# Optimization experiments

Hardware: AMD Instinct MI355X
Metric: run time of the kernel (lower is better)

The kernel has to match this reference:

```python
import jax, jax.numpy as jnp
import numpy as np

B, D, G, L = 8, 128, 2048, 24
GF = G // 2 + 1  # rfft bins
EPS = 1e-5


def setup_inputs() -> dict:
    key = jax.random.key(0)
    ks = jax.random.split(key, 6)
    x = jax.random.normal(ks[0], (B, D, G), dtype=jnp.float32)
    Phi_f = jax.random.normal(ks[1], (L, GF), dtype=jnp.float32) * 0.1
    Theta = jax.random.normal(ks[2], (L, D, D), dtype=jnp.float32) * (1.0 / np.sqrt(D))
    ln_gamma = jnp.ones((D,), dtype=jnp.float32)
    ln_beta = jnp.zeros((D,), dtype=jnp.float32)
    fc1_w = jax.random.normal(ks[3], (2 * D, D), dtype=jnp.float32) * (1.0 / np.sqrt(D))
    fc1_b = jnp.zeros((2 * D,), dtype=jnp.float32)
    fc2_w = jax.random.normal(ks[4], (D, 2 * D), dtype=jnp.float32) * (1.0 / np.sqrt(2 * D))
    fc2_b = jnp.zeros((D,), dtype=jnp.float32)
    return {
        'x': x, 'Phi_f': Phi_f, 'Theta': Theta,
        'ln_gamma': ln_gamma, 'ln_beta': ln_beta,
        'fc1_w': fc1_w, 'fc1_b': fc1_b, 'fc2_w': fc2_w, 'fc2_b': fc2_b,
    }


def reference(x, Phi_f, Theta, ln_gamma, ln_beta, fc1_w, fc1_b, fc2_w, fc2_b):
    # x: (B, D, G). LayerNorm over the lifting (channel) dim D.
    mean = jnp.mean(x, axis=1, keepdims=True)
    var = jnp.var(x, axis=1, keepdims=True)
    z = (x - mean) * jax.lax.rsqrt(var + EPS)
    z = z * ln_gamma[None, :, None] + ln_beta[None, :, None]

    # Spectral convolution with each Hilbert filter.
    Xf = jnp.fft.rfft(z, axis=-1)                       # (B, D, GF) complex
    Uf = Xf[:, :, None, :] * jnp.conj(Phi_f)[None, None]  # (B, D, L, GF)
    U = jnp.fft.irfft(Uf, n=G, axis=-1)                 # (B, D, L, G)

    # Per-filter channel mixing then reduction over filters:
    # einsum('bdln,lhd->bhln') followed by sum over l, fused:
    S = jnp.einsum('bdlg,lhd->bhg', U, Theta)           # (B, D, G)

    # Pointwise MLP (Conv1d kernel_size=1 == channel matmul).
    H = jnp.einsum('hd,bdg->bhg', fc1_w, S) + fc1_b[None, :, None]
    H = jax.nn.gelu(H, approximate=False)
    out = jnp.einsum('dh,bhg->bdg', fc2_w, H) + fc2_b[None, :, None]
    return x + out
```

## Files before the change

kernel.cpp:

```cpp
#include <hip/hip_runtime.h>
#include <math.h>


#define B_   8
#define D_   128
#define G_   2048
#define L_   24
#define GF_  1025
#define BD_  1024
#define DD_  16384
#define GH_  1024
#define CF_  1026
#define MF_  1088
#define NF_  2048

#define PA_CV0 256
#define PA_TT0 322
#define PA_WF0 578
#define PA_WI0 1666
#define PA_END 2690

#define G1_NB  544
#define G1_END 4768

typedef __attribute__((ext_vector_type(8))) short  short8v;
typedef __attribute__((ext_vector_type(4))) float  float4v;

union FU { float f; unsigned int u; };
union V8 { short8v v; ushort u[8]; };
union V4 { uint2 p; ushort u[4]; };

static __device__ __forceinline__ float bf2f(ushort h) {
    FU v; v.u = ((unsigned int)h) << 16; return v.f;
}
static __device__ __forceinline__ ushort f2bf(float f) {
    FU v; v.f = f;
    unsigned int r = v.u + 0x7fffu + ((v.u >> 16) & 1u);
    return (ushort)(r >> 16);
}
static __device__ __forceinline__ void async16(const void* g, void* l) {
    __builtin_amdgcn_global_load_lds(
        (const __attribute__((address_space(1))) void*)g,
        (__attribute__((address_space(3))) void*)l, 16, 0, 0);
}
static __device__ __forceinline__ int is_f32(const unsigned int* graw) {
    return graw[0] == 0x3F800000u;
}

__global__ __launch_bounds__(256) void k_pre(
        const void* __restrict__ x_raw,  const void* __restrict__ th_raw,
        const unsigned int* __restrict__ graw, const void* __restrict__ be_raw,
        const void* __restrict__ w1_raw, const void* __restrict__ b1_raw,
        const void* __restrict__ w2_raw, const void* __restrict__ b2_raw,
        ushort* __restrict__ z,  ushort* __restrict__ wf,
        ushort* __restrict__ wi, ushort* __restrict__ thT,
        ushort* __restrict__ w1c, ushort* __restrict__ b1c,
        ushort* __restrict__ w2c, ushort* __restrict__ b2c) {
    __shared__ ushort T[L_][72];
    __shared__ float red[2][256];
    __shared__ float mi[2][64];
    int bid = blockIdx.x, tid = threadIdx.x;

    if (bid < PA_CV0) {
        int fl = is_f32(graw);
        int b  = bid >> 5;
        int g0 = (bid & 31) * 64;
        int gi = tid & 63, dq = tid >> 6;
        int g  = g0 + gi;
        int d0 = dq * 32;
        float vals[32];
        float s = 0.f, ss = 0.f;
        if (fl) {
            const float* xp = (const float*)x_raw + (size_t)(b * D_ + d0) * G_ + g;
            #pragma unroll 8
            for (int d = 0; d < 32; ++d) {
                float v = xp[(size_t)d * G_];
                vals[d] = v; s += v; ss += v * v;
            }
        } else {
            const ushort* xp = (const ushort*)x_raw + (size_t)(b * D_ + d0) * G_ + g;
            #pragma unroll 8
            for (int d = 0; d < 32; ++d) {
                float v = bf2f(xp[(size_t)d * G_]);
                vals[d] = v; s += v; ss += v * v;
            }
        }
        red[0][tid] = s; red[1][tid] = ss;
        __syncthreads();
        if (tid < 64) {
            float S  = red[0][tid] + red[0][tid + 64] + red[0][tid + 128] +
                       red[0][tid + 192];
            float SS = red[1][tid] + red[1][tid + 64] + red[1][tid + 128] +
                       red[1][tid + 192];
            float mean = S * (1.f / D_);
            float var  = SS * (1.f / D_) - mean * mean;
            mi[0][tid] = mean;
            mi[1][tid] = rsqrtf(var + 1e-5f);
        }
        __syncthreads();
        float mean = mi[0][gi], inv = mi[1][gi];
        ushort* zp = z + (size_t)(g & 1) * (BD_ * GH_) +
                     (size_t)(b * D_ + d0) * GH_ + (g >> 1);
        if (fl) {
            const float* gp = (const float*)graw + d0;
            const float* bp = (const float*)be_raw + d0;
            #pragma unroll 8
            for (int d = 0; d < 32; ++d) {
                float o = (vals[d] - mean) * inv * gp[d] + bp[d];
                zp[(size_t)d * GH_] = f2bf(o);
            }
        } else {
            const ushort* gp = (const ushort*)graw + d0;
            const ushort* bp = (const ushort*)be_raw + d0;
            #pragma unroll 8
            for (int d = 0; d < 32; ++d) {
                float o = (vals[d] - mean) * inv * bf2f(gp[d]) + bf2f(bp[d]);
                zp[(size_t)d * GH_] = f2bf(o);
            }
        }
    } else if (bid < PA_TT0) {
        int fl = is_f32(graw);
        int lb = bid - PA_CV0;
        const void* src; ushort* dst; int n, rel;
        if (lb < 32)       { src = w1_raw; dst = w1c; n = 32768; rel = lb; }
        else if (lb == 32) { src = b1_raw; dst = b1c; n = 256;   rel = 0; }
        else if (lb < 65)  { src = w2_raw; dst = w2c; n = 32768; rel = lb - 33; }
        else               { src = b2_raw; dst = b2c; n = 128;   rel = 0; }
        int i0 = rel * 1024 + tid * 4;
        if (fl) {
            const float* s = (const float*)src;
            #pragma unroll
            for (int j = 0; j < 4; ++j) {
                int k = i0 + j;
                if (k < n) dst[k] = f2bf(s[k]);
            }
        } else {
            const ushort* s = (const ushort*)src;
            #pragma unroll
            for (int j = 0; j < 4; ++j) {
                int k = i0 + j;
                if (k < n) dst[k] = s[k];
            }
        }
    } else if (bid < PA_WF0) {
        int fl = is_f32(graw);
        int hd0 = (bid - PA_TT0) * 64;
        if (tid < 192) {
            int l = tid >> 3, c8 = tid & 7;
            V8 o;
            if (fl) {
                const float* tp = (const float*)th_raw + (size_t)l * DD_ +
                                  hd0 + c8 * 8;
                float4v a0 = *(const float4v*)tp;
                float4v a1 = *(const float4v*)(tp + 4);
                #pragma unroll
                for (int j = 0; j < 4; ++j) {
                    o.u[j] = f2bf(a0[j]); o.u[4 + j] = f2bf(a1[j]);
                }
            } else {
                o.v = *(const short8v*)((const ushort*)th_raw +
                                        (size_t)l * DD_ + hd0 + c8 * 8);
            }
            *(short8v*)&T[l][c8 * 8] = o.v;
        }
        __syncthreads();
        int hdl = tid & 63, part = tid >> 6;
        V8 o;
        #pragma unroll
        for (int j = 0; j < 8; ++j) {
            int l = part * 8 + j;
            o.u[j] = (l < L_) ? T[l][hdl] : (ushort)0;
        }
        *(short8v*)(thT + (size_t)(hd0 + hdl) * 32 + part * 8) = o.v;
    } else if (bid < PA_WI0) {
        int c  = bid - PA_WF0;
        int g0 = tid * 4;
        V4 v;
        if (c >= CF_) {
            #pragma unroll
            for (int j = 0; j < 4; ++j) v.u[j] = 0;
        } else {
            int f = c >> 1, im = c & 1;
            #pragma unroll
            for (int j = 0; j < 4; ++j) {
                int g = g0 + j;
                int r = (f * g) & (GH_ - 1);
                float th = (float)r * 6.135923151542565e-3f;
                v.u[j] = f2bf(im ? -__sinf(th) : __cosf(th));
            }
        }
        *(uint2*)(wf + (size_t)c * GH_ + g0) = v.p;
    } else {
        int g = bid - PA_WI0;
        for (int ch = tid; ch < MF_ / 8; ch += 256) {
            int c0 = ch * 8;
            V8 v;
            #pragma unroll
            for (int j = 0; j < 8; ++j) {
                int c = c0 + j;
                if (c >= CF_) { v.u[j] = 0; continue; }
                int f = c >> 1, im = c & 1;
                float a = (f == 0 || f == GH_ / 2) ? (1.f / 2048.f)
                                                   : (1.f / 1024.f);
                int r = (f * g) & (GH_ - 1);
                float th = (float)r * 6.135923151542565e-3f;
                v.u[j] = f2bf(im ? -a * __sinf(th) : a * __cosf(th));
            }
            *(short8v*)(wi + (size_t)g * MF_ + c0) = v.v;
        }
    }
}

__global__ __launch_bounds__(256, 4) void k_g1(
        const ushort* __restrict__ wf, const ushort* __restrict__ z,
        ushort* __restrict__ zft,
        const void* __restrict__ phi_raw, const unsigned int* __restrict__ graw,
        const ushort* __restrict__ thT, ushort* __restrict__ M) {
    __shared__ ushort As[2][64 * 64];
    __shared__ ushort Bs[2][64 * 64];
    __shared__ ushort Aph[16][40];
    int bid = blockIdx.x, tid = threadIdx.x;
    int w = tid >> 6, lane = tid & 63;
    int lr = lane & 15, q = lane >> 4;

    if (bid < G1_NB) {
        int m0 = (bid >> 5) * 64;
        int n0 = (bid & 31) * 64;
        int wm = (w & 1) * 32, wn = (w >> 1) * 32;
        int rl = lane >> 3, c8 = (lane & 7) ^ rl;
        int t0 = w * 2, t1 = w * 2 + 1;
        const ushort* gA0 = wf + (size_t)(m0 + t0 * 8 + rl) * GH_ + c8 * 8;
        const ushort* gA1 = wf + (size_t)(m0 + t1 * 8 + rl) * GH_ + c8 * 8;
        const ushort* gB0 = z  + (size_t)(n0 + t0 * 8 + rl) * GH_ + c8 * 8;
        const ushort* gB1 = z  + (size_t)(n0 + t1 * 8 + rl) * GH_ + c8 * 8;

        float4v acc00 = {0.f,0.f,0.f,0.f}, acc01 = {0.f,0.f,0.f,0.f};
        float4v acc10 = {0.f,0.f,0.f,0.f}, acc11 = {0.f,0.f,0.f,0.f};

        async16(gA0, &As[0][t0 * 512]);
        async16(gA1, &As[0][t1 * 512]);
        async16(gB0, &Bs[0][t0 * 512]);
        async16(gB1, &Bs[0][t1 * 512]);
        __syncthreads();

        int buf = 0;
        for (int k0 = 0; k0 < GH_; k0 += 64) {
            if (k0 + 64 < GH_) {
                int nb = buf ^ 1;
                async16(gA0 + k0 + 64, &As[nb][t0 * 512]);
                async16(gA1 + k0 + 64, &As[nb][t1 * 512]);
                async16(gB0 + k0 + 64, &Bs[nb][t0 * 512]);
                async16(gB1 + k0 + 64, &Bs[nb][t1 * 512]);
            }
            const ushort* Ab = &As[buf][0];
            const ushort* Bb = &Bs[buf][0];
            #pragma unroll
            for (int s = 0; s < 2; ++s) {
                int cs = s * 4 + q;
                int ra0 = wm + lr, ra1 = wm + 16 + lr;
                int rb0 = wn + lr, rb1 = wn + 16 + lr;
                short8v a0 = *(const short8v*)(Ab + ra0 * 64 + ((cs ^ (ra0 & 7)) << 3));
                short8v a1 = *(const short8v*)(Ab + ra1 * 64 + ((cs ^ (ra1 & 7)) << 3));
                short8v b0 = *(const short8v*)(Bb + rb0 * 64 + ((cs ^ (rb0 & 7)) << 3));
                short8v b1 = *(const short8v*)(Bb + rb1 * 64 + ((cs ^ (rb1 & 7)) << 3));
                acc00 = __builtin_amdgcn_mfma_f32_16x16x32_bf16(a0, b0, acc00, 0, 0, 0);
                acc01 = __builtin_amdgcn_mfma_f32_16x16x32_bf16(a0, b1, acc01, 0, 0, 0);
                acc10 = __builtin_amdgcn_mfma_f32_16x16x32_bf16(a1, b0, acc10, 0, 0, 0);
                acc11 = __builtin_amdgcn_mfma_f32_16x16x32_bf16(a1, b1, acc11, 0, 0, 0);
            }
            __syncthreads();
            buf ^= 1;
        }

        float4v accs[2][2] = { { acc00, acc01 }, { acc10, acc11 } };
        #pragma unroll
        for (int i = 0; i < 2; ++i)
            #pragma unroll
            for (int j = 0; j < 2; ++j) {
                int col = n0 + wn + j * 16 + lr;
                int row = m0 + wm + i * 16 + q * 4;
                #pragma unroll
                for (int r = 0; r < 4; ++r)
                    zft[(size_t)(row + r) * NF_ + col] = f2bf(accs[i][j][r]);
            }
    } else {
        int bb  = bid - G1_NB;
        int f0  = (bb >> 6) * 16;
        int hd0 = (bb & 63) * 256;
        int isf = is_f32(graw);
        #pragma unroll
        for (int rep = 0; rep < 2; ++rep) {
            int idx = rep * 256 + tid;
            int fl = idx >> 5, l = idx & 31;
            int f = f0 + fl;
            ushort v = 0;
            if (l < L_ && f < GF_)
                v = isf ? f2bf(((const float*)phi_raw)[(size_t)l * GF_ + f])
                        : ((const ushort*)phi_raw)[(size_t)l * GF_ + f];
            Aph[fl][l] = v;
        }
        __syncthreads();
        short8v a = *(const short8v*)&Aph[lr][q * 8];
        #pragma unroll
        for (int t = 0; t < 4; ++t) {
            int n = hd0 + (w * 4 + t) * 16 + lr;
            short8v b = *(const short8v*)(thT + (size_t)n * 32 + q * 8);
            float4v c = {0.f, 0.f, 0.f, 0.f};
            c = __builtin_amdgcn_mfma_f32_16x16x32_bf16(a, b, c, 0, 0, 0);
            #pragma unroll
            for (int r = 0; r < 4; ++r) {
                int f = f0 + q * 4 + r;
                if (f < GF_) M[(size_t)f * DD_ + n] = f2bf(c[r]);
            }
        }
    }
}

__global__ __launch_bounds__(256, 2) void k_mix3(const ushort* __restrict__ zft,
                                                 const ushort* __restrict__ M,
                                                 ushort* __restrict__ sft) {
    int fp  = blockIdx.x;
    int fb  = GH_ - fp;
    int tid = threadIdx.x;
    int w = tid >> 6, lane = tid & 63;
    int lr = lane & 15, q = lane >> 4;
    int cc = lr >> 3, bb = lr & 7;

    float ang = (float)fp * 3.0679615757712823e-3f;
    float wr  = cosf(ang), sn = sinf(ang);
    float wi_ = -sn;
    float wsig = cc ? wi_ : -wi_;
    float cbv  = cc ? wr  : -wr;
    float asgn = cc ? -1.f : 1.f;

    const ushort* rc = zft + (size_t)(2 * fp + cc) * NF_;
    const ushort* ro = zft + (size_t)(2 * fp + (cc ^ 1)) * NF_;
    int colb = bb * 128 + q * 8;

    short8v aZ[4], aZb[4];
    #pragma unroll
    for (int s = 0; s < 4; ++s) {
        int col = colb + s * 32;
        V8 aU, bU, oU;
        aU.v = *(const short8v*)(rc + col);
        bU.v = *(const short8v*)(rc + BD_ + col);
        oU.v = *(const short8v*)(ro + BD_ + col);
        V8 tz, tb;
        #pragma unroll
        for (int j = 0; j < 8; ++j) {
            float av = bf2f(aU.u[j]), bv = bf2f(bU.u[j]), bo = bf2f(oU.u[j]);
            float zz = fmaf(wsig, bo, fmaf(wr, bv, av));
            float zb = fmaf(cbv, bv, fmaf(wi_, bo, asgn * av));
            tz.u[j] = f2bf(zz); tb.u[j] = f2bf(zb);
        }
        aZ[s] = tz.v; aZb[s] = tb.v;
    }

    const ushort* Mf = M + (size_t)fp * DD_;
    const ushort* Mb = M + (size_t)fb * DD_;
    #pragma unroll
    for (int n = 0; n < 2; ++n) {
        int nt = 2 * w + n;
        float4v c1 = {0.f, 0.f, 0.f, 0.f};
        float4v c2 = {0.f, 0.f, 0.f, 0.f};
        #pragma unroll
        for (int s = 0; s < 4; ++s) {
            short8v b1 = *(const short8v*)(Mf + (size_t)(nt * 16 + lr) * D_ +
                                           s * 32 + q * 8);
            short8v b2 = *(const short8v*)(Mb + (size_t)(nt * 16 + lr) * D_ +
                                           s * 32 + q * 8);
            c1 = __builtin_amdgcn_mfma_f32_16x16x32_bf16(aZ[s],  b1, c1, 0, 0, 0);
            c2 = __builtin_amdgcn_mfma_f32_16x16x32_bf16(aZb[s], b2, c2, 0, 0, 0);
        }
        #pragma unroll
        for (int r = 0; r < 4; ++r) {
            int p   = q * 4 + r;
            int c2i = p >> 3, b2 = p & 7;
            float sgm = c2i ? -1.f : 1.f;
            float se  = c1[r] + sgm * c2[r];
            float sop = c1[r] - sgm * c2[r];
            float pp  = __shfl_xor(sop, 32);
            float tsg = c2i ? sn : -sn;
            float so  = fmaf(tsg, pp, sop * wr);
            size_t rowo = (size_t)(2 * fp + c2i) * NF_;
            int colh = b2 * 128 + nt * 16 + lr;
            sft[rowo + colh]       = f2bf(se);
            sft[rowo + BD_ + colh] = f2bf(so);
        }
    }
}

__global__ __launch_bounds__(256, 4) void k_gemm64t(const ushort* __restrict__ A,
                                                    const ushort* __restrict__ Bm,
                                                    ushort* __restrict__ C,
                                                    int K, int lda, int ldb,
                                                    int ldc, int kv) {
    __shared__ ushort As[2][64 * 64];
    __shared__ ushort Bs[2][64 * 64];
    int tid = threadIdx.x;
    int m0 = blockIdx.x * 64, n0 = blockIdx.y * 64;
    int w = tid >> 6, lane = tid & 63;
    int lr = lane & 15, q = lane >> 4;
    int wm = (w & 1) * 32, wn = (w >> 1) * 32;

    int rl = lane >> 3, c8 = (lane & 7) ^ rl;
    int t0 = w * 2, t1 = w * 2 + 1;
    const ushort* gA0 = A + (size_t)(m0 + t0 * 8 + rl) * lda + c8 * 8;
    const ushort* gA1 = A + (size_t)(m0 + t1 * 8 + rl) * lda + c8 * 8;

    int br = tid >> 2;
    int bc = tid & 3;

    float4v acc00 = {0.f,0.f,0.f,0.f}, acc01 = {0.f,0.f,0.f,0.f};
    float4v acc10 = {0.f,0.f,0.f,0.f}, acc11 = {0.f,0.f,0.f,0.f};

    async16(gA0, &As[0][t0 * 512]);
    async16(gA1, &As[0][t1 * 512]);
    {
        V8 u0, u1;
        if (br < kv) {
            const ushort* gb = Bm + (size_t)br * ldb + n0 + bc * 16;
            u0.v = *(const short8v*)gb;
            u1.v = *(const short8v*)(gb + 8);
        } else {
            #pragma unroll
            for (int j = 0; j < 8; ++j) { u0.u[j] = 0; u1.u[j] = 0; }
        }
        #pragma unroll
        for (int j = 0; j < 8; ++j) {
            int n = bc * 16 + j;
            Bs[0][n * 64 + ((((br >> 3) ^ (n & 7)) << 3) | (br & 7))] = u0.u[j];
        }
        #pragma unroll
        for (int j = 0; j < 8; ++j) {
            int n = bc * 16 + 8 + j;
            Bs[0][n * 64 + ((((br >> 3) ^ (n & 7)) << 3) | (br & 7))] = u1.u[j];
        }
    }
    __syncthreads();

    int buf = 0;
    for (int k0 = 0; k0 < K; k0 += 64) {
        V8 u0, u1;
        bool more = (k0 + 64 < K);
        if (more) {
            int nb = buf ^ 1;
            async16(gA0 + k0 + 64, &As[nb][t0 * 512]);
            async16(gA1 + k0 + 64, &As[nb][t1 * 512]);
            int kr = k0 + 64 + br;
            if (kr < kv) {
                const ushort* gb = Bm + (size_t)kr * ldb + n0 + bc * 16;
                u0.v = *(const short8v*)gb;
                u1.v = *(const short8v*)(gb + 8);
            } else {
                #pragma unroll
                for (int j = 0; j < 8; ++j) { u0.u[j] = 0; u1.u[j] = 0; }
            }
        }
        const ushort* Ab = &As[buf][0];
        const ushort* Bb = &Bs[buf][0];
        #pragma unroll
        for (int s = 0; s < 2; ++s) {
            int cs = s * 4 + q;
            int ra0 = wm + lr, ra1 = wm + 16 + lr;
            int rb0 = wn + lr, rb1 = wn + 16 + lr;
            short8v a0 = *(const short8v*)(Ab + ra0 * 64 + ((cs ^ (ra0 & 7)) << 3));
            short8v a1 = *(const short8v*)(Ab + ra1 * 64 + ((cs ^ (ra1 & 7)) << 3));
            short8v b0 = *(const short8v*)(Bb + rb0 * 64 + ((cs ^ (rb0 & 7)) << 3));
            short8v b1 = *(const short8v*)(Bb + rb1 * 64 + ((cs ^ (rb1 & 7)) << 3));
            acc00 = __builtin_amdgcn_mfma_f32_16x16x32_bf16(a0, b0, acc00, 0, 0, 0);
            acc01 = __builtin_amdgcn_mfma_f32_16x16x32_bf16(a0, b1, acc01, 0, 0, 0);
            acc10 = __builtin_amdgcn_mfma_f32_16x16x32_bf16(a1, b0, acc10, 0, 0, 0);
            acc11 = __builtin_amdgcn_mfma_f32_16x16x32_bf16(a1, b1, acc11, 0, 0, 0);
        }
        __syncthreads();
        if (more) {
            int nb = buf ^ 1;
            #pragma unroll
            for (int j = 0; j < 8; ++j) {
                int n = bc * 16 + j;
                Bs[nb][n * 64 + ((((br >> 3) ^ (n & 7)) << 3) | (br & 7))] = u0.u[j];
            }
            #pragma unroll
            for (int j = 0; j < 8; ++j) {
                int n = bc * 16 + 8 + j;
                Bs[nb][n * 64 + ((((br >> 3) ^ (n & 7)) << 3) | (br & 7))] = u1.u[j];
            }
        }
        __syncthreads();
        buf ^= 1;
    }

    float4v accs[2][2] = { { acc00, acc01 }, { acc10, acc11 } };
    #pragma unroll
    for (int i = 0; i < 2; ++i)
        #pragma unroll
        for (int j = 0; j < 2; ++j) {
            int col = n0 + wn + j * 16 + lr;
            int row = m0 + wm + i * 16 + q * 4;
            #pragma unroll
            for (int r = 0; r < 4; ++r)
                C[(size_t)(row + r) * ldc + col] = f2bf(accs[i][j][r]);
        }
}

#define MLPG 32
__global__ __launch_bounds__(256, 2) void k_mlp3(const ushort* __restrict__ ST,
                                                 const void* __restrict__ x0,
                                                 const ushort* __restrict__ w1,
                                                 const ushort* __restrict__ b1,
                                                 const ushort* __restrict__ w2,
                                                 const ushort* __restrict__ b2,
                                                 const unsigned int* __restrict__ graw,
                                                 void* __restrict__ outv) {
    __shared__ ushort Sb[MLPG][136];
    __shared__ ushort Hb[MLPG][264];
    __shared__ float  Ob[128][36];
    int g0 = blockIdx.x * MLPG, b = blockIdx.y;
    int tid = threadIdx.x;
    {
        int col = tid >> 3, seg = tid & 7;
        int g = g0 + col;
        const ushort* sp = ST + (size_t)(g >> 1) * NF_ + (g & 1) * BD_ +
                           b * D_ + seg * 16;
        short8v s0 = *(const short8v*)(sp);
        short8v s1 = *(const short8v*)(sp + 8);
        *(short8v*)&Sb[col][seg * 16]     = s0;
        *(short8v*)&Sb[col][seg * 16 + 8] = s1;
    }
    __syncthreads();
    int w = tid >> 6, lane = tid & 63;
    int lr = lane & 15, q = lane >> 4;
    int nt = w & 1, mh = w >> 1;

    {
        float4v acc[8];
        #pragma unroll
        for (int i = 0; i < 8; ++i) { float4v zz = {0.f,0.f,0.f,0.f}; acc[i] = zz; }
        #pragma unroll
        for (int ks = 0; ks < 4; ++ks) {
            short8v bf = *(const short8v*)&Sb[nt * 16 + lr][ks * 32 + q * 8];
            #pragma unroll
            for (int i = 0; i < 8; ++i) {
                int mt = mh * 8 + i;
                short8v af = *(const short8v*)(w1 + (size_t)(mt * 16 + lr) * D_ +
                                               ks * 32 + q * 8);
                acc[i] = __builtin_amdgcn_mfma_f32_16x16x32_bf16(af, bf, acc[i], 0, 0, 0);
            }
        }
        #pragma unroll
        for (int i = 0; i < 8; ++i) {
            int h0 = (mh * 8 + i) * 16 + q * 4;
            V4 hv;
            #pragma unroll
            for (int r = 0; r < 4; ++r) {
                float v = acc[i][r] + bf2f(b1[h0 + r]);
                v = 0.5f * v * (1.f + erff(v * 0.70710678118f));
                hv.u[r] = f2bf(v);
            }
            *(uint2*)&Hb[nt * 16 + lr][h0] = hv.p;
        }
    }
    __syncthreads();
    {
        float4v acc2[4];
        #pragma unroll
        for (int j = 0; j < 4; ++j) { float4v zz = {0.f,0.f,0.f,0.f}; acc2[j] = zz; }
        #pragma unroll
        for (int ks = 0; ks < 8; ++ks) {
            short8v bf = *(const short8v*)&Hb[nt * 16 + lr][ks * 32 + q * 8];
            #pragma unroll
            for (int j = 0; j < 4; ++j) {
                int mt2 = mh * 4 + j;
                short8v af = *(const short8v*)(w2 + (size_t)(mt2 * 16 + lr) * (2 * D_) +
                                               ks * 32 + q * 8);
                acc2[j] = __builtin_amdgcn_mfma_f32_16x16x32_bf16(af, bf, acc2[j], 0, 0, 0);
            }
        }
        int col = nt * 16 + lr;
        #pragma unroll
        for (int j = 0; j < 4; ++j) {
            int d0 = (mh * 4 + j) * 16 + q * 4;
            #pragma unroll
            for (int r = 0; r < 4; ++r)
                Ob[d0 + r][col] = acc2[j][r] + bf2f(b2[d0 + r]);
        }
    }
    __syncthreads();
    {
        int fl = is_f32(graw);
        if (fl) {
            #pragma unroll
            for (int p = 0; p < 4; ++p) {
                int idx = p * 256 + tid;
                int d = idx >> 3, c4 = (idx & 7) * 4;
                float4v o = *(const float4v*)&Ob[d][c4];
                size_t gidx = ((size_t)(b * D_ + d)) * G_ + g0 + c4;
                float4v xv = *(const float4v*)((const float*)x0 + gidx);
                float4v ov;
                #pragma unroll
                for (int k = 0; k < 4; ++k) ov[k] = o[k] + xv[k];
                *(float4v*)((float*)outv + gidx) = ov;
            }
        } else {
            #pragma unroll
            for (int p = 0; p < 4; ++p) {
                int idx = p * 256 + tid;
                int d = idx >> 3, c4 = (idx & 7) * 4;
                float4v o = *(const float4v*)&Ob[d][c4];
                size_t gidx = ((size_t)(b * D_ + d)) * G_ + g0 + c4;
                V4 xv; xv.p = *(const uint2*)((const ushort*)x0 + gidx);
                V4 ov;
                #pragma unroll
                for (int k = 0; k < 4; ++k) ov.u[k] = f2bf(o[k] + bf2f(xv.u[k]));
                *(uint2*)((ushort*)outv + gidx) = ov.p;
            }
        }
    }
}

extern "C" void kernel_launch(void* const* d_in, const int* in_sizes, int n_in,
                              void* d_out, int out_size, void* d_ws, size_t ws_size,
                              hipStream_t stream) {
    char* base = (char*)d_ws;
    ushort* z    = (ushort*)(base);
    ushort* wf   = (ushort*)(base + 4194304);
    ushort* sft  = (ushort*)(base);
    ushort* zft  = (ushort*)(base + 13107200);
    ushort* st   = (ushort*)(base + 13107200);
    ushort* w1c  = (ushort*)(base + 27050048);
    ushort* b1c  = (ushort*)(base + 27115584);
    ushort* w2c  = (ushort*)(base + 27116096);
    ushort* b2c  = (ushort*)(base + 27181632);
    ushort* Mm   = (ushort*)(base + 27182592);
    ushort* wi   = (ushort*)(base + 60769792);
    ushort* thT  = (ushort*)(base + 69420544);

    const unsigned int* graw = (const unsigned int*)d_in[3];

    k_pre    <<<dim3(PA_END), 256, 0, stream>>>(
        d_in[0], d_in[2], graw, d_in[4], d_in[5], d_in[6], d_in[7], d_in[8],
        z, wf, wi, thT, w1c, b1c, w2c, b2c);
    k_g1     <<<dim3(G1_END), 256, 0, stream>>>(wf, z, zft, d_in[1], graw,
                                                thT, Mm);
    k_mix3   <<<dim3(513), 256, 0, stream>>>(zft, Mm, sft);
    k_gemm64t<<<dim3(GH_ / 64, NF_ / 64), 256, 0, stream>>>(
        wi, sft, st, MF_, MF_, NF_, NF_, CF_);
    k_mlp3   <<<dim3(G_ / MLPG, B_), 256, 0, stream>>>(st, d_in[0], w1c, b1c,
                                                       w2c, b2c, graw, d_out);
}
```

Baseline: 160.8 us.

## Switch DFT decomposition from radix-2 to radix-4 polyphase split

The sequence is now split into four interleaved phases of 512 points instead of two of 1024. The dense DFT-by-matmul in k_g1 and the inverse in k_gemm64t therefore run with K of 512 and about 576 rather than 1024 and 1088, which cuts their MAC count roughly in half. k_mix3 now does radix-4 twiddle recombination, applies four per-frequency mixing matrices (fp, 512-fp, 512+fp, 1024-fp), and writes four output phases. The cost is more twiddle arithmetic and more shuffles in the mix kernel, plus new sign and index bookkeeping that could introduce errors.

```diff
diff --git a/kernel.cpp b/kernel.cpp
--- a/kernel.cpp
+++ b/kernel.cpp
@@ -9,19 +9,19 @@
 #define GF_  1025
 #define BD_  1024
 #define DD_  16384
-#define GH_  1024
-#define CF_  1026
-#define MF_  1088
-#define NF_  2048
+#define GQ_  512
+#define CF4_ 514
+#define MF4_ 576
+#define NF4_ 4096
 
 #define PA_CV0 256
 #define PA_TT0 322
 #define PA_WF0 578
-#define PA_WI0 1666
-#define PA_END 2690
-
-#define G1_NB  544
-#define G1_END 4768
+#define PA_WI0 1154
+#define PA_END 1666
+
+#define G1_NB  576
+#define G1_END 4800
 
 typedef __attribute__((ext_vector_type(8))) short  short8v;
 typedef __attribute__((ext_vector_type(4))) float  float4v;
@@ -99,15 +99,15 @@
         }
         __syncthreads();
         float mean = mi[0][gi], inv = mi[1][gi];
-        ushort* zp = z + (size_t)(g & 1) * (BD_ * GH_) +
-                     (size_t)(b * D_ + d0) * GH_ + (g >> 1);
+        ushort* zp = z + (size_t)(g & 3) * (BD_ * GQ_) +
+                     (size_t)(b * D_ + d0) * GQ_ + (g >> 2);
         if (fl) {
             const float* gp = (const float*)graw + d0;
             const float* bp = (const float*)be_raw + d0;
             #pragma unroll 8
             for (int d = 0; d < 32; ++d) {
                 float o = (vals[d] - mean) * inv * gp[d] + bp[d];
-                zp[(size_t)d * GH_] = f2bf(o);
+                zp[(size_t)d * GQ_] = f2bf(o);
             }
         } else {
             const ushort* gp = (const ushort*)graw + d0;
@@ -115,7 +115,7 @@
             #pragma unroll 8
             for (int d = 0; d < 32; ++d) {
                 float o = (vals[d] - mean) * inv * bf2f(gp[d]) + bf2f(bp[d]);
-                zp[(size_t)d * GH_] = f2bf(o);
+                zp[(size_t)d * GQ_] = f2bf(o);
             }
         }
     } else if (bid < PA_TT0) {
@@ -173,40 +173,42 @@
         }
         *(short8v*)(thT + (size_t)(hd0 + hdl) * 32 + part * 8) = o.v;
     } else if (bid < PA_WI0) {
-        int c  = bid - PA_WF0;
-        int g0 = tid * 4;
-        V4 v;
-        if (c >= CF_) {
-            #pragma unroll
-            for (int j = 0; j < 4; ++j) v.u[j] = 0;
-        } else {
-            int f = c >> 1, im = c & 1;
-            #pragma unroll
-            for (int j = 0; j < 4; ++j) {
-                int g = g0 + j;
-                int r = (f * g) & (GH_ - 1);
-                float th = (float)r * 6.135923151542565e-3f;
-                v.u[j] = f2bf(im ? -__sinf(th) : __cosf(th));
-            }
-        }
-        *(uint2*)(wf + (size_t)c * GH_ + g0) = v.p;
+        int c = bid - PA_WF0;
+        if (tid < 128) {
+            int g0 = tid * 4;
+            V4 v;
+            if (c >= CF4_) {
+                #pragma unroll
+                for (int j = 0; j < 4; ++j) v.u[j] = 0;
+            } else {
+                int f = c >> 1, im = c & 1;
+                #pragma unroll
+                for (int j = 0; j < 4; ++j) {
+                    int g = g0 + j;
+                    int r = (f * g) & (GQ_ - 1);
+                    float th = (float)r * 1.2271846303085130e-2f;
+                    v.u[j] = f2bf(im ? -__sinf(th) : __cosf(th));
+                }
+            }
+            *(uint2*)(wf + (size_t)c * GQ_ + g0) = v.p;
+        }
     } else {
         int g = bid - PA_WI0;
-        for (int ch = tid; ch < MF_ / 8; ch += 256) {
+        for (int ch = tid; ch < MF4_ / 8; ch += 256) {
             int c0 = ch * 8;
             V8 v;
             #pragma unroll
             for (int j = 0; j < 8; ++j) {
                 int c = c0 + j;
-                if (c >= CF_) { v.u[j] = 0; continue; }
+                if (c >= CF4_) { v.u[j] = 0; continue; }
                 int f = c >> 1, im = c & 1;
-                float a = (f == 0 || f == GH_ / 2) ? (1.f / 2048.f)
-                                                   : (1.f / 1024.f);
-                int r = (f * g) & (GH_ - 1);
-                float th = (float)r * 6.135923151542565e-3f;
+                float a = (f == 0 || f == GQ_ / 2) ? 4.8828125e-4f
+                                                   : 9.765625e-4f;
+                int r = (f * g) & (GQ_ - 1);
+                float th = (float)r * 1.2271846303085130e-2f;
                 v.u[j] = f2bf(im ? -a * __sinf(th) : a * __cosf(th));
             }
-            *(short8v*)(wi + (size_t)g * MF_ + c0) = v.v;
+            *(short8v*)(wi + (size_t)g * MF4_ + c0) = v.v;
         }
     }
 }
@@ -224,15 +226,15 @@
     int lr = lane & 15, q = lane >> 4;
 
     if (bid < G1_NB) {
-        int m0 = (bid >> 5) * 64;
-        int n0 = (bid & 31) * 64;
+        int m0 = (bid >> 6) * 64;
+        int n0 = (bid & 63) * 64;
         int wm = (w & 1) * 32, wn = (w >> 1) * 32;
         int rl = lane >> 3, c8 = (lane & 7) ^ rl;
         int t0 = w * 2, t1 = w * 2 + 1;
-        const ushort* gA0 = wf + (size_t)(m0 + t0 * 8 + rl) * GH_ + c8 * 8;
-        const ushort* gA1 = wf + (size_t)(m0 + t1 * 8 + rl) * GH_ + c8 * 8;
-        const ushort* gB0 = z  + (size_t)(n0 + t0 * 8 + rl) * GH_ + c8 * 8;
-        const ushort* gB1 = z  + (size_t)(n0 + t1 * 8 + rl) * GH_ + c8 * 8;
+        const ushort* gA0 = wf + (size_t)(m0 + t0 * 8 + rl) * GQ_ + c8 * 8;
+        const ushort* gA1 = wf + (size_t)(m0 + t1 * 8 + rl) * GQ_ + c8 * 8;
+        const ushort* gB0 = z  + (size_t)(n0 + t0 * 8 + rl) * GQ_ + c8 * 8;
+        const ushort* gB1 = z  + (size_t)(n0 + t1 * 8 + rl) * GQ_ + c8 * 8;
 
         float4v acc00 = {0.f,0.f,0.f,0.f}, acc01 = {0.f,0.f,0.f,0.f};
         float4v acc10 = {0.f,0.f,0.f,0.f}, acc11 = {0.f,0.f,0.f,0.f};
@@ -244,8 +246,8 @@
         __syncthreads();
 
         int buf = 0;
-        for (int k0 = 0; k0 < GH_; k0 += 64) {
-            if (k0 + 64 < GH_) {
+        for (int k0 = 0; k0 < GQ_; k0 += 64) {
+            if (k0 + 64 < GQ_) {
                 int nb = buf ^ 1;
                 async16(gA0 + k0 + 64, &As[nb][t0 * 512]);
                 async16(gA1 + k0 + 64, &As[nb][t1 * 512]);
@@ -281,7 +283,7 @@
                 int row = m0 + wm + i * 16 + q * 4;
                 #pragma unroll
                 for (int r = 0; r < 4; ++r)
-                    zft[(size_t)(row + r) * NF_ + col] = f2bf(accs[i][j][r]);
+                    zft[(size_t)(row + r) * NF4_ + col] = f2bf(accs[i][j][r]);
             }
     } else {
         int bb  = bid - G1_NB;
@@ -319,74 +321,117 @@
 __global__ __launch_bounds__(256, 2) void k_mix3(const ushort* __restrict__ zft,
                                                  const ushort* __restrict__ M,
                                                  ushort* __restrict__ sft) {
-    int fp  = blockIdx.x;
-    int fb  = GH_ - fp;
+    int bx  = blockIdx.x;
+    int fp  = bx >> 1;
+    int hh  = bx & 1;
     int tid = threadIdx.x;
     int w = tid >> 6, lane = tid & 63;
     int lr = lane & 15, q = lane >> 4;
     int cc = lr >> 3, bb = lr & 7;
-
-    float ang = (float)fp * 3.0679615757712823e-3f;
-    float wr  = cosf(ang), sn = sinf(ang);
-    float wi_ = -sn;
-    float wsig = cc ? wi_ : -wi_;
-    float cbv  = cc ? wr  : -wr;
-    float asgn = cc ? -1.f : 1.f;
-
-    const ushort* rc = zft + (size_t)(2 * fp + cc) * NF_;
-    const ushort* ro = zft + (size_t)(2 * fp + (cc ^ 1)) * NF_;
+    int ntg = hh * 4 + w;
+
+    float a1 = (float)fp * 3.0679615757712823e-3f;
+    float C1 = cosf(a1),        S1 = sinf(a1);
+    float C2 = cosf(2.f * a1),  S2 = sinf(2.f * a1);
+    float C3 = cosf(3.f * a1),  S3 = sinf(3.f * a1);
+
+    float P01 = cc ? -S1 :  C1,  Q01 = cc ?  C1 :  S1;
+    float P02 = cc ? -S2 :  C2,  Q02 = cc ?  C2 :  S2;
+    float P03 = cc ? -S3 :  C3,  Q03 = cc ?  C3 :  S3;
+    float P11 = cc ? -C1 :  S1,  Q11 = cc ? -S1 : -C1;
+    float P12 = cc ? -S2 : -C2,  Q12 = cc ?  C2 : -S2;
+    float P13 = cc ?  C3 : -S3,  Q13 = cc ?  S3 :  C3;
+    float P21 = cc ? -C1 : -S1,  Q21 = cc ? -S1 :  C1;
+    float P22 = cc ?  S2 : -C2,  Q22 = cc ? -C2 : -S2;
+    float P23 = cc ?  C3 :  S3,  Q23 = cc ?  S3 : -C3;
+    float P31 = cc ? -S1 : -C1,  Q31 = cc ?  C1 : -S1;
+    float P32 = cc ?  S2 :  C2,  Q32 = cc ? -C2 :  S2;
+    float P33 = cc ? -S3 : -C3,  Q33 = cc ?  C3 : -S3;
+
+    const ushort* r0 = zft + (size_t)(2 * fp) * NF4_;
+    const ushort* r1 = r0 + NF4_;
     int colb = bb * 128 + q * 8;
 
-    short8v aZ[4], aZb[4];
+    short8v aZ[4][4];
     #pragma unroll
     for (int s = 0; s < 4; ++s) {
         int col = colb + s * 32;
-        V8 aU, bU, oU;
-        aU.v = *(const short8v*)(rc + col);
-        bU.v = *(const short8v*)(rc + BD_ + col);
-        oU.v = *(const short8v*)(ro + BD_ + col);
-        V8 tz, tb;
-        #pragma unroll
-        for (int j = 0; j < 8; ++j) {
-            float av = bf2f(aU.u[j]), bv = bf2f(bU.u[j]), bo = bf2f(oU.u[j]);
-            float zz = fmaf(wsig, bo, fmaf(wr, bv, av));
-            float zb = fmaf(cbv, bv, fmaf(wi_, bo, asgn * av));
-            tz.u[j] = f2bf(zz); tb.u[j] = f2bf(zb);
-        }
-        aZ[s] = tz.v; aZb[s] = tb.v;
-    }
-
-    const ushort* Mf = M + (size_t)fp * DD_;
-    const ushort* Mb = M + (size_t)fb * DD_;
+        V8 R0, I0, R1, I1, R2, I2, R3, I3;
+        R0.v = *(const short8v*)(r0 + col);
+        I0.v = *(const short8v*)(r1 + col);
+        R1.v = *(const short8v*)(r0 + 1024 + col);
+        I1.v = *(const short8v*)(r1 + 1024 + col);
+        R2.v = *(const short8v*)(r0 + 2048 + col);
+        I2.v = *(const short8v*)(r1 + 2048 + col);
+        R3.v = *(const short8v*)(r0 + 3072 + col);
+        I3.v = *(const short8v*)(r1 + 3072 + col);
+        V8 t0, t1, t2, t3;
+        #pragma unroll
+        for (int e = 0; e < 8; ++e) {
+            float x0 = bf2f(R0.u[e]), y0 = bf2f(I0.u[e]);
+            float x1 = bf2f(R1.u[e]), y1 = bf2f(I1.u[e]);
+            float x2 = bf2f(R2.u[e]), y2 = bf2f(I2.u[e]);
+            float x3 = bf2f(R3.u[e]), y3 = bf2f(I3.u[e]);
+            float e0p = cc ?  y0 : x0;
+            float e0m = cc ? -y0 : x0;
+            float z0 = e0p, z1 = e0m, z2 = e0p, z3 = e0m;
+            z0 = fmaf(P01, x1, z0); z0 = fmaf(Q01, y1, z0);
+            z0 = fmaf(P02, x2, z0); z0 = fmaf(Q02, y2, z0);
+            z0 = fmaf(P03, x3, z0); z0 = fmaf(Q03, y3, z0);
+            z1 = fmaf(P11, x1, z1); z1 = fmaf(Q11, y1, z1);
+            z1 = fmaf(P12, x2, z1); z1 = fmaf(Q12, y2, z1);
+            z1 = fmaf(P13, x3, z1); z1 = fmaf(Q13, y3, z1);
+            z2 = fmaf(P21, x1, z2); z2 = fmaf(Q21, y1, z2);
+            z2 = fmaf(P22, x2, z2); z2 = fmaf(Q22, y2, z2);
+            z2 = fmaf(P23, x3, z2); z2 = fmaf(Q23, y3, z2);
+            z3 = fmaf(P31, x1, z3); z3 = fmaf(Q31, y1, z3);
+            z3 = fmaf(P32, x2, z3); z3 = fmaf(Q32, y2, z3);
+            z3 = fmaf(P33, x3, z3); z3 = fmaf(Q33, y3, z3);
+            t0.u[e] = f2bf(z0); t1.u[e] = f2bf(z1);
+            t2.u[e] = f2bf(z2); t3.u[e] = f2bf(z3);
+        }
+        aZ[0][s] = t0.v; aZ[1][s] = t1.v; aZ[2][s] = t2.v; aZ[3][s] = t3.v;
+    }
+
+    int fk0 = fp, fk1 = 512 - fp, fk2 = 512 + fp, fk3 = 1024 - fp;
+    const ushort* Mp[4] = { M + (size_t)fk0 * DD_, M + (size_t)fk1 * DD_,
+                            M + (size_t)fk2 * DD_, M + (size_t)fk3 * DD_ };
+    float4v acc[4];
     #pragma unroll
-    for (int n = 0; n < 2; ++n) {
-        int nt = 2 * w + n;
-        float4v c1 = {0.f, 0.f, 0.f, 0.f};
-        float4v c2 = {0.f, 0.f, 0.f, 0.f};
+    for (int k = 0; k < 4; ++k) {
+        float4v c = {0.f, 0.f, 0.f, 0.f};
         #pragma unroll
         for (int s = 0; s < 4; ++s) {
-            short8v b1 = *(const short8v*)(Mf + (size_t)(nt * 16 + lr) * D_ +
-                                           s * 32 + q * 8);
-            short8v b2 = *(const short8v*)(Mb + (size_t)(nt * 16 + lr) * D_ +
-                                           s * 32 + q * 8);
-            c1 = __builtin_amdgcn_mfma_f32_16x16x32_bf16(aZ[s],  b1, c1, 0, 0, 0);
-            c2 = __builtin_amdgcn_mfma_f32_16x16x32_bf16(aZb[s], b2, c2, 0, 0, 0);
-        }
-        #pragma unroll
-        for (int r = 0; r < 4; ++r) {
-            int p   = q * 4 + r;
-            int c2i = p >> 3, b2 = p & 7;
-            float sgm = c2i ? -1.f : 1.f;
-            float se  = c1[r] + sgm * c2[r];
-            float sop = c1[r] - sgm * c2[r];
-            float pp  = __shfl_xor(sop, 32);
-            float tsg = c2i ? sn : -sn;
-            float so  = fmaf(tsg, pp, sop * wr);
-            size_t rowo = (size_t)(2 * fp + c2i) * NF_;
-            int colh = b2 * 128 + nt * 16 + lr;
-            sft[rowo + colh]       = f2bf(se);
-            sft[rowo + BD_ + colh] = f2bf(so);
-        }
+            short8v bfr = *(const short8v*)(Mp[k] + (size_t)(ntg * 16 + lr) * D_ +
+                                            s * 32 + q * 8);
+            c = __builtin_amdgcn_mfma_f32_16x16x32_bf16(aZ[k][s], bfr, c, 0, 0, 0);
+        }
+        acc[k] = c;
+    }
+
+    #pragma unroll
+    for (int e = 0; e < 4; ++e) {
+        int p   = q * 4 + e;
+        int c2i = p >> 3, cb = p & 7;
+        float sg = c2i ? -1.f : 1.f;
+        float u0 = acc[0][e], u1 = acc[1][e], u2 = acc[2][e], u3 = acc[3][e];
+        float p1 = __shfl_xor(u1, 32);
+        float p2 = __shfl_xor(u2, 32);
+        float U0 = u0 + u2 + sg * (u1 + u3);
+        float U1 = u0 - sg * p2 - sg * u3 - p1;
+        float U2 = u0 - u2 + sg * (u3 - u1);
+        float U3 = u0 + sg * p2 - sg * u3 + p1;
+        float U1p = __shfl_xor(U1, 32);
+        float U2p = __shfl_xor(U2, 32);
+        float U3p = __shfl_xor(U3, 32);
+        float T1 = fmaf(-sg * S1, U1p, C1 * U1);
+        float T2 = fmaf(-sg * S2, U2p, C2 * U2);
+        float T3 = fmaf(-sg * S3, U3p, C3 * U3);
+        size_t base = (size_t)(2 * fp + c2i) * NF4_ + cb * 128 + ntg * 16 + lr;
+        sft[base]          = f2bf(U0);
+        sft[base + 1024]   = f2bf(T1);
+        sft[base + 2048]   = f2bf(T2);
+        sft[base + 3072]   = f2bf(T3);
     }
 }
 
@@ -521,7 +566,7 @@
     {
         int col = tid >> 3, seg = tid & 7;
         int g = g0 + col;
-        const ushort* sp = ST + (size_t)(g >> 1) * NF_ + (g & 1) * BD_ +
+        const ushort* sp = ST + (size_t)(g >> 2) * NF4_ + (g & 3) * BD_ +
                            b * D_ + seg * 16;
         short8v s0 = *(const short8v*)(sp);
         short8v s1 = *(const short8v*)(sp + 8);
@@ -643,9 +688,9 @@
         z, wf, wi, thT, w1c, b1c, w2c, b2c);
     k_g1     <<<dim3(G1_END), 256, 0, stream>>>(wf, z, zft, d_in[1], graw,
                                                 thT, Mm);
-    k_mix3   <<<dim3(513), 256, 0, stream>>>(zft, Mm, sft);
-    k_gemm64t<<<dim3(GH_ / 64, NF_ / 64), 256, 0, stream>>>(
-        wi, sft, st, MF_, MF_, NF_, NF_, CF_);
+    k_mix3   <<<dim3(514), 256, 0, stream>>>(zft, Mm, sft);
+    k_gemm64t<<<dim3(GQ_ / 64, NF4_ / 64), 256, 0, stream>>>(
+        wi, sft, st, MF4_, MF4_, NF4_, NF4_, CF4_);
     k_mlp3   <<<dim3(G_ / MLPG, B_), 256, 0, stream>>>(st, d_in[0], w1c, b1c,
                                                        w2c, b2c, graw, d_out);
 }
```

Measured after the change: 157.5 us. -2.0%, faster.
